# Optimization experiments

Measured on AMD Instinct MI355X. Metric: run time of the kernel, lower is better.

## Reference

```python
import jax, jax.numpy as jnp
import numpy as np

HALF_FEATURE_NUMEL = 49152  # 12 pieces * 64 squares * 64 king buckets
INTER_DIM = 768             # factorizer collapses king bucket: i % 768


def setup_inputs() -> dict:
    key = jax.random.key(0)
    k1, k2, k3, k4 = jax.random.split(key, 4)
    N = 16384
    nnz = N * 32  # ~32 active features per position
    batch_idx = jnp.sort(jax.random.randint(k1, (nnz,), 0, N, dtype=jnp.int64 if jax.config.read('jax_enable_x64') else jnp.int32))
    active_idx = jax.random.randint(k2, (nnz,), 0, HALF_FEATURE_NUMEL)
    values = jax.random.uniform(k3, (nnz,), dtype=jnp.float32)
    # factorization table self.f = [func(i) for i in range(half_feature_numel)]
    f_table = jnp.arange(HALF_FEATURE_NUMEL) % INTER_DIM
    weights = jax.random.normal(k4, (INTER_DIM, 256), dtype=jnp.float32) * 0.01
    return {"batch_idx": batch_idx, "active_idx": active_idx, "values": values,
            "f_table": f_table, "weights": weights, "N": N}


def reference(batch_idx, active_idx, values, f_table, weights, N):
    # gather: remap active feature ids through factorization table
    factored = f_table[active_idx]                      # [nnz]
    inter_dim = weights.shape[0]
    # scatter-sum duplicates into dense [N, inter_dim] (== sparse COO .to_dense())
    x = jnp.zeros((N, inter_dim), dtype=values.dtype)
    x = x.at[batch_idx, factored].add(values)
    # dense matmul with factored weights
    return x @ weights                                  # [N, output_dim]
```

## Files before the change

### kernel.cpp

```cpp
#include <hip/hip_runtime.h>
#include <hip/hip_fp16.h>


#define OUT_COLS 256
#define WAVES_PER_BLOCK 4
#define BLOCK_THREADS (WAVES_PER_BLOCK * 64)
#define NW (768 * 256)

__global__ __launch_bounds__(256)
void build_kernel(const int* __restrict__ batch_idx,
                  const int* __restrict__ active_idx,
                  const float* __restrict__ values,
                  const int* __restrict__ f_table,
                  const float* __restrict__ weights,
                  int* __restrict__ offsets,
                  unsigned* __restrict__ pairs,
                  __half* __restrict__ wh,
                  int nnz, int N)
{
    const int k = blockIdx.x * 256 + threadIdx.x;
    if (k < NW) wh[k] = __float2half(weights[k]);
    if (k >= nnz) return;
    const int r  = batch_idx[k];
    const int rp = (k == 0) ? -1 : batch_idx[k - 1];
    for (int row = rp + 1; row <= r; ++row) offsets[row] = k;
    if (k == nnz - 1)
        for (int row = r + 1; row <= N; ++row) offsets[row] = nnz;
    const unsigned f = (unsigned)f_table[active_idx[k]];
    pairs[k] = (f << 16) | (unsigned)__half_as_ushort(__float2half(values[k]));
}

__global__ __launch_bounds__(BLOCK_THREADS, 8)
void gemm_kernel(const int* __restrict__ offsets,
                 const unsigned* __restrict__ pairs,
                 const __half* __restrict__ wh,
                 float* __restrict__ out, int N)
{
    const int lane = threadIdx.x & 63;
    const int row  = blockIdx.x * WAVES_PER_BLOCK + (threadIdx.x >> 6);
    if (row >= N) return;

    const int start = __builtin_amdgcn_readfirstlane(offsets[row]);
    const int end   = __builtin_amdgcn_readfirstlane(offsets[row + 1]);

    const __half2 zero = __float2half2_rn(0.0f);
    __half2 acc0 = zero, acc1 = zero, acc2 = zero, acc3 = zero;

    const __half* __restrict__ wbase = wh + ((lane & 31) << 3);
    const bool lo_half = (lane < 32);

    for (int k = start; k < end; k += 16) {
        unsigned p[16];
#pragma unroll
        for (int j = 0; j < 16; ++j) {
            const unsigned raw = pairs[k + j];
            p[j] = (k + j < end) ? raw : 0u;
        }
        uint4 w[8];
#pragma unroll
        for (int b = 0; b < 8; ++b) {
            const int f0 = (int)(p[2 * b] >> 16);
            const int f1 = (int)(p[2 * b + 1] >> 16);
            const int f  = lo_half ? f0 : f1;
            w[b] = *(const uint4*)(wbase + (f << 8));
        }
#pragma unroll
        for (int b = 0; b < 8; ++b) {
            unsigned vv0 = p[2 * b] & 0xffffu;       vv0 |= vv0 << 16;
            unsigned vv1 = p[2 * b + 1] & 0xffffu;   vv1 |= vv1 << 16;
            const unsigned vvu = lo_half ? vv0 : vv1;
            const __half2 vv = *(const __half2*)&vvu;
            const __half2* w2 = (const __half2*)&w[b];
            acc0 = __hfma2(w2[0], vv, acc0);
            acc1 = __hfma2(w2[1], vv, acc1);
            acc2 = __hfma2(w2[2], vv, acc2);
            acc3 = __hfma2(w2[3], vv, acc3);
        }
    }

    __half2 accs[4] = {acc0, acc1, acc2, acc3};
#pragma unroll
    for (int i = 0; i < 4; ++i) {
        int a = *(const int*)&accs[i];
        const int b = __shfl_xor(a, 32);
        accs[i] = __hadd2(accs[i], *(const __half2*)&b);
    }
    if (lo_half) {
        float4 o0, o1;
        o0.x = __low2float(accs[0]); o0.y = __high2float(accs[0]);
        o0.z = __low2float(accs[1]); o0.w = __high2float(accs[1]);
        o1.x = __low2float(accs[2]); o1.y = __high2float(accs[2]);
        o1.z = __low2float(accs[3]); o1.w = __high2float(accs[3]);
        float* orow = out + row * OUT_COLS + (lane << 3);
        *(float4*)orow = o0;
        *(float4*)(orow + 4) = o1;
    }
}

__global__ __launch_bounds__(256, 8)
void fallback_kernel(const int* __restrict__ batch_idx,
                     const int* __restrict__ active_idx,
                     const float* __restrict__ values,
                     const int* __restrict__ f_table,
                     const float* __restrict__ weights,
                     float* __restrict__ out,
                     int nnz, int N)
{
    const int wave = threadIdx.x >> 6;
    const int lane = threadIdx.x & 63;
    const int row  = blockIdx.x * 4 + wave;
    if (row >= N) return;

    int lo1 = 0, hi1 = nnz, lo2 = 0, hi2 = nnz;
    while ((lo1 < hi1) | (lo2 < hi2)) {
        if (lo1 < hi1) { int m = (lo1 + hi1) >> 1; if (batch_idx[m] < row) lo1 = m + 1; else hi1 = m; }
        if (lo2 < hi2) { int m = (lo2 + hi2) >> 1; if (batch_idx[m] < row + 1) lo2 = m + 1; else hi2 = m; }
    }
    float4 acc = make_float4(0.f, 0.f, 0.f, 0.f);
    const float* __restrict__ wcol = weights + (lane << 2);
    for (int base = lo1; base < lo2; base += 64) {
        const int cnt = min(lo2 - base, 64);
        float v_l = 0.f; int f_l = 0;
        if (lane < cnt) { const int k = base + lane; v_l = values[k]; f_l = f_table[active_idx[k]]; }
        for (int j = 0; j < cnt; ++j) {
            const float v = __shfl(v_l, j);
            const int   f = __shfl(f_l, j);
            const float4 w = *(const float4*)(wcol + f * OUT_COLS);
            acc.x = fmaf(v, w.x, acc.x);
            acc.y = fmaf(v, w.y, acc.y);
            acc.z = fmaf(v, w.z, acc.z);
            acc.w = fmaf(v, w.w, acc.w);
        }
    }
    *(float4*)(out + row * OUT_COLS + (lane << 2)) = acc;
}

extern "C" void kernel_launch(void* const* d_in, const int* in_sizes, int n_in,
                              void* d_out, int out_size, void* d_ws, size_t ws_size,
                              hipStream_t stream) {
    const int*   batch_idx  = (const int*)d_in[0];
    const int*   active_idx = (const int*)d_in[1];
    const float* values     = (const float*)d_in[2];
    const int*   f_table    = (const int*)d_in[3];
    const float* weights    = (const float*)d_in[4];
    float*       out        = (float*)d_out;

    const int nnz = in_sizes[0];
    const int N   = out_size / OUT_COLS;

    const size_t off_bytes = (size_t)(N + 1) * sizeof(int);
    const size_t wh_off    = (off_bytes + 15) & ~(size_t)15;
    const size_t pairs_off = (wh_off + (size_t)NW * 2 + 15) & ~(size_t)15;
    const size_t need      = pairs_off + (size_t)nnz * sizeof(unsigned) + 64;

    const int grid_rows = (N + WAVES_PER_BLOCK - 1) / WAVES_PER_BLOCK;

    if (ws_size >= need) {
        int*      offsets = (int*)d_ws;
        __half*   wh      = (__half*)((char*)d_ws + wh_off);
        unsigned* pairs   = (unsigned*)((char*)d_ws + pairs_off);

        const int work = (nnz > NW) ? nnz : NW;
        build_kernel<<<(work + 255) / 256, 256, 0, stream>>>(
            batch_idx, active_idx, values, f_table, weights,
            offsets, pairs, wh, nnz, N);
        gemm_kernel<<<grid_rows, BLOCK_THREADS, 0, stream>>>(offsets, pairs, wh, out, N);
    } else {
        fallback_kernel<<<grid_rows, 256, 0, stream>>>(
            batch_idx, active_idx, values, f_table, weights, out, nnz, N);
    }
}
```

Baseline: 89.28 us.

## Load row pairs once per wave and broadcast via ds_bpermute

The gemm kernel now loads both row offsets with one per-lane load plus shuffles. It also fetches up to 64 (feature, value) pairs with a single coalesced load, one per lane. The per-pair data is then distributed to the two half-waves via ds_bpermute, instead of every lane redundantly loading 16 pairs per iteration. Rows with more than 64 entries fall through to a scalar tail loop, and the workspace padding is enlarged to cover the over-read of 64 pairs past the row start.

```diff
diff --git a/kernel.cpp b/kernel.cpp
--- a/kernel.cpp
+++ b/kernel.cpp
@@ -40,42 +40,49 @@
     const int row  = blockIdx.x * WAVES_PER_BLOCK + (threadIdx.x >> 6);
     if (row >= N) return;
 
-    const int start = __builtin_amdgcn_readfirstlane(offsets[row]);
-    const int end   = __builtin_amdgcn_readfirstlane(offsets[row + 1]);
+    const int off_v = offsets[row + (lane & 1)];
+    const int start = __shfl(off_v, 0);
+    const int end   = __shfl(off_v, 1);
+    const int cnt   = end - start;
+
+    const unsigned praw = pairs[start + lane];
+
+    const int vhi  = lane >> 5;
+    const int vhi4 = vhi << 2;
+    const __half* __restrict__ wcol = wh + ((lane & 31) << 3);
 
     const __half2 zero = __float2half2_rn(0.0f);
     __half2 acc0 = zero, acc1 = zero, acc2 = zero, acc3 = zero;
 
-    const __half* __restrict__ wbase = wh + ((lane & 31) << 3);
-    const bool lo_half = (lane < 32);
+    const int nb = (min(cnt, 64) + 1) >> 1;
 
-    for (int k = start; k < end; k += 16) {
-        unsigned p[16];
-#pragma unroll
-        for (int j = 0; j < 16; ++j) {
-            const unsigned raw = pairs[k + j];
-            p[j] = (k + j < end) ? raw : 0u;
-        }
-        uint4 w[8];
-#pragma unroll
-        for (int b = 0; b < 8; ++b) {
-            const int f0 = (int)(p[2 * b] >> 16);
-            const int f1 = (int)(p[2 * b + 1] >> 16);
-            const int f  = lo_half ? f0 : f1;
-            w[b] = *(const uint4*)(wbase + (f << 8));
-        }
-#pragma unroll
-        for (int b = 0; b < 8; ++b) {
-            unsigned vv0 = p[2 * b] & 0xffffu;       vv0 |= vv0 << 16;
-            unsigned vv1 = p[2 * b + 1] & 0xffffu;   vv1 |= vv1 << 16;
-            const unsigned vvu = lo_half ? vv0 : vv1;
-            const __half2 vv = *(const __half2*)&vvu;
-            const __half2* w2 = (const __half2*)&w[b];
-            acc0 = __hfma2(w2[0], vv, acc0);
-            acc1 = __hfma2(w2[1], vv, acc1);
-            acc2 = __hfma2(w2[2], vv, acc2);
-            acc3 = __hfma2(w2[3], vv, acc3);
-        }
+#pragma unroll 4
+    for (int b = 0; b < nb; ++b) {
+        const int idx = 2 * b + vhi;
+        int pb = __builtin_amdgcn_ds_bpermute(vhi4 + (b << 3), (int)praw);
+        pb = (idx < cnt) ? pb : 0;
+        const unsigned up = (unsigned)pb;
+        const uint4 wv = *(const uint4*)((const char*)wcol + ((up >> 16) << 9));
+        unsigned vvu = (up & 0xffffu) | (up << 16);
+        const __half2 vv = *(const __half2*)&vvu;
+        const __half2* w2 = (const __half2*)&wv;
+        acc0 = __hfma2(w2[0], vv, acc0);
+        acc1 = __hfma2(w2[1], vv, acc1);
+        acc2 = __hfma2(w2[2], vv, acc2);
+        acc3 = __hfma2(w2[3], vv, acc3);
+    }
+
+    for (int k = start + 64; k < end; ++k) {
+        unsigned p = pairs[k];
+        if (vhi) p = 0;
+        const uint4 wv = *(const uint4*)((const char*)wcol + ((p >> 16) << 9));
+        unsigned vvu = (p & 0xffffu) | (p << 16);
+        const __half2 vv = *(const __half2*)&vvu;
+        const __half2* w2 = (const __half2*)&wv;
+        acc0 = __hfma2(w2[0], vv, acc0);
+        acc1 = __hfma2(w2[1], vv, acc1);
+        acc2 = __hfma2(w2[2], vv, acc2);
+        acc3 = __hfma2(w2[3], vv, acc3);
     }
 
     __half2 accs[4] = {acc0, acc1, acc2, acc3};
@@ -85,13 +92,13 @@
         const int b = __shfl_xor(a, 32);
         accs[i] = __hadd2(accs[i], *(const __half2*)&b);
     }
-    if (lo_half) {
+    if (vhi == 0) {
         float4 o0, o1;
         o0.x = __low2float(accs[0]); o0.y = __high2float(accs[0]);
         o0.z = __low2float(accs[1]); o0.w = __high2float(accs[1]);
         o1.x = __low2float(accs[2]); o1.y = __high2float(accs[2]);
         o1.z = __low2float(accs[3]); o1.w = __high2float(accs[3]);
-        float* orow = out + row * OUT_COLS + (lane << 3);
+        float* orow = out + (size_t)row * OUT_COLS + ((lane & 31) << 3);
         *(float4*)orow = o0;
         *(float4*)(orow + 4) = o1;
     }
@@ -119,10 +126,10 @@
     float4 acc = make_float4(0.f, 0.f, 0.f, 0.f);
     const float* __restrict__ wcol = weights + (lane << 2);
     for (int base = lo1; base < lo2; base += 64) {
-        const int cnt = min(lo2 - base, 64);
+        const int c = min(lo2 - base, 64);
         float v_l = 0.f; int f_l = 0;
-        if (lane < cnt) { const int k = base + lane; v_l = values[k]; f_l = f_table[active_idx[k]]; }
-        for (int j = 0; j < cnt; ++j) {
+        if (lane < c) { const int k = base + lane; v_l = values[k]; f_l = f_table[active_idx[k]]; }
+        for (int j = 0; j < c; ++j) {
             const float v = __shfl(v_l, j);
             const int   f = __shfl(f_l, j);
             const float4 w = *(const float4*)(wcol + f * OUT_COLS);
@@ -151,7 +158,7 @@
     const size_t off_bytes = (size_t)(N + 1) * sizeof(int);
     const size_t wh_off    = (off_bytes + 15) & ~(size_t)15;
     const size_t pairs_off = (wh_off + (size_t)NW * 2 + 15) & ~(size_t)15;
-    const size_t need      = pairs_off + (size_t)nnz * sizeof(unsigned) + 64;
+    const size_t need      = pairs_off + (size_t)nnz * sizeof(unsigned) + 256;
 
     const int grid_rows = (N + WAVES_PER_BLOCK - 1) / WAVES_PER_BLOCK;
 
```

Result: no change. 90.67 us (+1.6%).
